# Kernel optimization log

Measured on AMD Instinct MI355X. Metric: run time of the kernel, lower is better.

Reference implementation:

```python
import jax, jax.numpy as jnp
import numpy as np
import math

SLIDING_WINDOW = 1024  # matches init kwarg

def setup_inputs() -> dict:
    key = jax.random.key(0)
    ks = jax.random.split(key, 6)
    B, S, Hq, Hkv, D = 1, 2048, 32, 8, 128
    NUM_PAGES, STRIDE = 300, 16
    q = jax.random.normal(ks[0], (B, S, Hq, D), dtype=jnp.float32)
    k = jax.random.normal(ks[1], (B, S, Hkv, D), dtype=jnp.float32)
    v = jax.random.normal(ks[2], (B, S, Hkv, D), dtype=jnp.float32)
    sink = jax.random.normal(ks[3], (Hq,), dtype=jnp.float32)
    cache_state = jnp.zeros((NUM_PAGES, STRIDE, 2, Hkv, D), dtype=jnp.float32)
    seq_block_ids = jax.random.randint(ks[4], (B, S // STRIDE), 0, NUM_PAGES, dtype=jnp.int64)
    return {"q": q, "k": k, "v": v, "sink": sink,
            "cache_state": cache_state, "seq_block_ids": seq_block_ids}


def reference(q, k, v, sink, cache_state, seq_block_ids):
    B, S, Hq, D = q.shape
    Hkv = k.shape[2]
    stride = cache_state.shape[1]

    # --- paged cache write (prefill side effect) ---
    kv = jnp.stack([k, v], axis=2)                       # [B,S,2,Hkv,D]
    pages = kv.reshape(B * (S // stride), stride, 2, Hkv, D)
    _ = cache_state.at[seq_block_ids.reshape(-1)].set(pages)

    # --- decomposed attention: matmul + mask + softmax(+sink) + matmul ---
    rep = Hq // Hkv
    ke = jnp.repeat(k, rep, axis=2)                      # [B,S,Hq,D] (GQA expand)
    ve = jnp.repeat(v, rep, axis=2)
    scale = 1.0 / math.sqrt(D)
    scores = jnp.einsum('bihd,bjhd->bhij', q, ke) * scale  # [B,Hq,S,S]

    i = jnp.arange(S)[:, None]
    j = jnp.arange(S)[None, :]
    allowed = (j <= i) & (i - j < SLIDING_WINDOW)        # causal + sliding window
    neg = jnp.finfo(scores.dtype).min
    logits = jnp.where(allowed, scores, neg)

    # attention sink: extra per-head logit appended; contributes to denominator only
    sink_l = jnp.broadcast_to(sink[None, :, None, None], (B, Hq, S, 1))
    probs = jax.nn.softmax(jnp.concatenate([logits, sink_l], axis=-1), axis=-1)[..., :S]

    out = jnp.einsum('bhij,bjhd->bihd', probs, ve)       # [B,S,Hq,D]
    return out
```

## Files before the change

kernel.cpp:

```cpp
#include <hip/hip_runtime.h>
#include <hip/hip_bf16.h>


#define S_LEN 2048
#define DH    128
#define HQ    32
#define HKV   8
#define WIN   1024
#define BR    64
#define BC    32
#define NT    (S_LEN / BC)
#define FM    16.0f
#define TILE_CH 512

typedef unsigned short u16;
typedef __attribute__((ext_vector_type(8))) short  short8;
typedef __attribute__((ext_vector_type(4))) float  floatx4;
typedef __attribute__((ext_vector_type(4))) unsigned int uintx4;

__device__ __forceinline__ unsigned rne1(float a) {
    unsigned u = __float_as_uint(a);
    return (u + 0x7FFFu + ((u >> 16) & 1u)) >> 16;
}
__device__ __forceinline__ unsigned rne_pk(float a, float b) {
    return rne1(a) | (rne1(b) << 16);
}

__global__ __launch_bounds__(256) void pack_kv(const float* __restrict__ kg,
                                               const float* __restrict__ vg,
                                               u16* __restrict__ kp,
                                               u16* __restrict__ vtp)
{
    __shared__ float Vs[BC][DH + 1];
    const int b   = blockIdx.x;
    const int hk  = b >> 6;
    const int jt  = b & 63;
    const int tid = threadIdx.x;
    const int j0  = jt * BC;

    #pragma unroll
    for (int t = 0; t < 4; t++) {
        int idx = tid + t * 256;
        int j   = idx >> 5;
        int dc  = idx & 31;
        floatx4 f = *(const floatx4*)(vg + ((size_t)(j0 + j) * HKV + hk) * DH + dc * 4);
        Vs[j][dc * 4 + 0] = f[0]; Vs[j][dc * 4 + 1] = f[1];
        Vs[j][dc * 4 + 2] = f[2]; Vs[j][dc * 4 + 3] = f[3];
    }

    u16* kpt = kp + (size_t)b * TILE_CH * 8;
    #pragma unroll
    for (int t = 0; t < 2; t++) {
        int c = tid + t * 256;
        int row = c >> 4, cc = c & 15;
        const float* p = kg + ((size_t)(j0 + row) * HKV + hk) * DH + cc * 8;
        floatx4 f0 = *(const floatx4*)p;
        floatx4 f1 = *(const floatx4*)(p + 4);
        int pc = (row << 4) | (cc ^ (row & 7));
        *(uintx4*)(kpt + pc * 8) =
            (uintx4){rne_pk(f0[0], f0[1]), rne_pk(f0[2], f0[3]),
                     rne_pk(f1[0], f1[1]), rne_pk(f1[2], f1[3])};
    }
    __syncthreads();

    u16* vpt = vtp + (size_t)b * TILE_CH * 8;
    #pragma unroll
    for (int t = 0; t < 2; t++) {
        int q  = tid + t * 256;
        int dd = q >> 2, c = q & 3;
        unsigned w0 = rne_pk(Vs[c * 4 + 0][dd], Vs[c * 4 + 16][dd]);
        unsigned w1 = rne_pk(Vs[c * 4 + 1][dd], Vs[c * 4 + 17][dd]);
        unsigned w2 = rne_pk(Vs[c * 4 + 2][dd], Vs[c * 4 + 18][dd]);
        unsigned w3 = rne_pk(Vs[c * 4 + 3][dd], Vs[c * 4 + 19][dd]);
        int qp = (dd << 2) | (c ^ ((dd >> 2) & 3));
        *(uintx4*)(vpt + qp * 8) = (uintx4){w0, w1, w2, w3};
    }
}

__launch_bounds__(256, 4)
__global__ void fa_kernel(const float* __restrict__ qg,
                          const u16* __restrict__ kp,
                          const u16* __restrict__ vtp,
                          const float* __restrict__ sg,
                          float* __restrict__ outg)
{
    __shared__ __align__(16) u16 Kt[2][TILE_CH * 8];
    __shared__ __align__(16) u16 Vt[2][TILE_CH * 8];
    __shared__ __align__(16) u16 Pb[BR * 40];

    const int tid  = threadIdx.x;
    const int w    = tid >> 6;
    const int lane = tid & 63;
    const int quad = lane >> 4;
    const int l16  = lane & 15;

    const int bid  = blockIdx.x;
    const int hk   = bid & 7;
    const int idx  = bid >> 3;
    const int hrem = idx & 3;
    const int u5   = (idx >> 2) & 7;
    const int t4   = idx >> 5;
    const int qbt[4] = {u5, 15 - u5, 16 + u5, 31 - u5};
    const int qb   = qbt[t4];
    const int h    = hk * 4 + hrem;

    const int i0 = qb * BR;
    const int m0 = i0 + w * 16;

    short8 qf[4];
    {
        const float* qrow = qg + ((size_t)(m0 + l16) * HQ + h) * DH;
        #pragma unroll
        for (int kk = 0; kk < 4; kk++) {
            const float* p = qrow + kk * 32 + quad * 8;
            floatx4 f0 = *(const floatx4*)p;
            floatx4 f1 = *(const floatx4*)(p + 4);
            uintx4 u = (uintx4){rne_pk(f0[0], f0[1]), rne_pk(f0[2], f0[3]),
                                rne_pk(f1[0], f1[1]), rne_pk(f1[2], f1[3])};
            qf[kk] = *(short8*)&u;
        }
    }

    floatx4 acc[8];
    #pragma unroll
    for (int i = 0; i < 8; i++) acc[i] = (floatx4){0.f, 0.f, 0.f, 0.f};
    float l_part[4] = {0.f, 0.f, 0.f, 0.f};

    int c_r[4];
    #pragma unroll
    for (int r = 0; r < 4; r++) c_r[r] = m0 + quad * 4 + r - l16;

    int jlo = i0 - (WIN - 1); if (jlo < 0) jlo = 0;
    const int jt_lo = jlo >> 5;
    const int jt_hi = (i0 + BR - 1) >> 5;

    const float SC2 = 0.08838834764831845f * 1.4426950408889634f;

    const int ch0 = w * 64 + lane;
    auto stage = [&](int bb, int jt) {
        const u16* kpt = kp  + ((size_t)(hk * NT + jt)) * TILE_CH * 8;
        const u16* vpt = vtp + ((size_t)(hk * NT + jt)) * TILE_CH * 8;
        #pragma unroll
        for (int it = 0; it < 2; it++) {
            int ch = ch0 + it * 256;
            __builtin_amdgcn_global_load_lds(
                (const __attribute__((address_space(1))) unsigned*)(kpt + ch * 8),
                (__attribute__((address_space(3))) unsigned*)(&Kt[bb][ch * 8]), 16, 0, 0);
            __builtin_amdgcn_global_load_lds(
                (const __attribute__((address_space(1))) unsigned*)(vpt + ch * 8),
                (__attribute__((address_space(3))) unsigned*)(&Vt[bb][ch * 8]), 16, 0, 0);
        }
    };

    stage(0, jt_lo);
    int bb = 0;

    for (int jt = jt_lo; jt <= jt_hi; jt++) {
        const int j0 = jt << 5;

        __syncthreads();

        if (jt < jt_hi) stage(bb ^ 1, jt + 1);

        floatx4 sc[2];
        sc[0] = (floatx4){0.f, 0.f, 0.f, 0.f};
        sc[1] = (floatx4){0.f, 0.f, 0.f, 0.f};
        #pragma unroll
        for (int kk = 0; kk < 4; kk++) {
            #pragma unroll
            for (int n = 0; n < 2; n++) {
                int row = n * 16 + l16;
                int cc  = kk * 4 + quad;
                int pc  = (row << 4) | (cc ^ (row & 7));
                short8 kf = *(const short8*)(&Kt[bb][pc * 8]);
                sc[n] = __builtin_amdgcn_mfma_f32_16x16x32_bf16(qf[kk], kf, sc[n], 0, 0, 0);
            }
        }

        const int prow0 = w * 16 + quad * 4;
        const bool interior = (j0 + (BC - 1) <= i0) && (j0 >= i0 + BR - WIN);
        if (interior) {
            #pragma unroll
            for (int r = 0; r < 4; r++) {
                float p0 = exp2f(fmaf(sc[0][r], SC2, -FM));
                float p1 = exp2f(fmaf(sc[1][r], SC2, -FM));
                l_part[r] += p0 + p1;
                *(unsigned*)(&Pb[(prow0 + r) * 40 + l16 * 2]) = rne_pk(p0, p1);
            }
        } else {
            #pragma unroll
            for (int r = 0; r < 4; r++) {
                bool a0 = (j0 <= c_r[r]) && (j0 > c_r[r] - WIN);
                bool a1 = (j0 + 16 <= c_r[r]) && (j0 + 16 > c_r[r] - WIN);
                float p0 = a0 ? exp2f(fmaf(sc[0][r], SC2, -FM)) : 0.f;
                float p1 = a1 ? exp2f(fmaf(sc[1][r], SC2, -FM)) : 0.f;
                l_part[r] += p0 + p1;
                *(unsigned*)(&Pb[(prow0 + r) * 40 + l16 * 2]) = rne_pk(p0, p1);
            }
        }

        {
            short8 pf = *(const short8*)(&Pb[(w * 16 + l16) * 40 + quad * 8]);
            #pragma unroll
            for (int nf = 0; nf < 8; nf++) {
                int dd = nf * 16 + l16;
                int qp = (dd << 2) | (quad ^ ((dd >> 2) & 3));
                short8 vf = *(const short8*)(&Vt[bb][qp * 8]);
                acc[nf] = __builtin_amdgcn_mfma_f32_16x16x32_bf16(pf, vf, acc[nf], 0, 0, 0);
            }
        }
        bb ^= 1;
    }

    const float sk2 = exp2f(fmaf(sg[h], 1.4426950408889634f, -FM));
    float inv[4];
    #pragma unroll
    for (int r = 0; r < 4; r++) {
        float l = l_part[r];
        #pragma unroll
        for (int off = 1; off < 16; off <<= 1)
            l += __shfl_xor(l, off);
        inv[r] = 1.f / (l + sk2);
    }
    #pragma unroll
    for (int nf = 0; nf < 8; nf++) {
        int d = nf * 16 + l16;
        #pragma unroll
        for (int r = 0; r < 4; r++) {
            int ig = m0 + quad * 4 + r;
            outg[((size_t)ig * HQ + h) * DH + d] = acc[nf][r] * inv[r];
        }
    }
}

__launch_bounds__(256, 4)
__global__ void fa_fallback(const float* __restrict__ qg,
                            const float* __restrict__ kg,
                            const float* __restrict__ vg,
                            const float* __restrict__ sg,
                            float* __restrict__ outg)
{
    __shared__ __align__(16) u16 Kt[BC * DH];
    __shared__ __align__(16) u16 Vt[DH * BC];
    __shared__ __align__(16) u16 Pb[BR * 40];

    const int tid  = threadIdx.x;
    const int w    = tid >> 6;
    const int lane = tid & 63;
    const int quad = lane >> 4;
    const int l16  = lane & 15;

    const int qb = blockIdx.x / HQ;
    const int h  = blockIdx.x % HQ;
    const int hk = h >> 2;
    const int i0 = qb * BR;
    const int m0 = i0 + w * 16;

    short8 qf[4];
    {
        const float* qrow = qg + ((size_t)(m0 + l16) * HQ + h) * DH;
        #pragma unroll
        for (int kk = 0; kk < 4; kk++) {
            const float* p = qrow + kk * 32 + quad * 8;
            floatx4 f0 = *(const floatx4*)p;
            floatx4 f1 = *(const floatx4*)(p + 4);
            uintx4 u = (uintx4){rne_pk(f0[0], f0[1]), rne_pk(f0[2], f0[3]),
                                rne_pk(f1[0], f1[1]), rne_pk(f1[2], f1[3])};
            qf[kk] = *(short8*)&u;
        }
    }

    floatx4 acc[8];
    #pragma unroll
    for (int i = 0; i < 8; i++) acc[i] = (floatx4){0.f, 0.f, 0.f, 0.f};
    float l_part[4] = {0.f, 0.f, 0.f, 0.f};

    int jlo = i0 - (WIN - 1); if (jlo < 0) jlo = 0;
    const int jt_lo = jlo >> 5;
    const int jt_hi = (i0 + BR - 1) >> 5;
    const float SC2 = 0.08838834764831845f * 1.4426950408889634f;

    for (int jt = jt_lo; jt <= jt_hi; jt++) {
        const int j0 = jt << 5;
        __syncthreads();
        #pragma unroll
        for (int it = 0; it < 2; it++) {
            int g   = tid + 256 * it;
            int row = g >> 4, cc = g & 15;
            int pc  = (row << 4) | (cc ^ (row & 7));
            const float* kpp = kg + ((size_t)(j0 + row) * HKV + hk) * DH + cc * 8;
            floatx4 f0 = *(const floatx4*)kpp;
            floatx4 f1 = *(const floatx4*)(kpp + 4);
            *(uintx4*)(&Kt[pc * 8]) =
                (uintx4){rne_pk(f0[0], f0[1]), rne_pk(f0[2], f0[3]),
                         rne_pk(f1[0], f1[1]), rne_pk(f1[2], f1[3])};
        }
        #pragma unroll
        for (int it = 0; it < 2; it++) {
            int g  = tid + 256 * it;
            int d  = g & 127, jc = g >> 7;
            const float* vp = vg + ((size_t)(j0 + jc * 8) * HKV + hk) * DH + d;
            float e0 = vp[0 * HKV * DH], e1 = vp[1 * HKV * DH];
            float e2 = vp[2 * HKV * DH], e3 = vp[3 * HKV * DH];
            float e4 = vp[4 * HKV * DH], e5 = vp[5 * HKV * DH];
            float e6 = vp[6 * HKV * DH], e7 = vp[7 * HKV * DH];
            int pc = (d << 2) | (jc ^ ((d >> 2) & 3));
            *(uintx4*)(&Vt[pc * 8]) =
                (uintx4){rne_pk(e0, e1), rne_pk(e2, e3), rne_pk(e4, e5), rne_pk(e6, e7)};
        }
        __syncthreads();

        floatx4 sc[2];
        sc[0] = (floatx4){0.f, 0.f, 0.f, 0.f};
        sc[1] = (floatx4){0.f, 0.f, 0.f, 0.f};
        #pragma unroll
        for (int kk = 0; kk < 4; kk++) {
            #pragma unroll
            for (int n = 0; n < 2; n++) {
                int row = n * 16 + l16;
                int cc  = kk * 4 + quad;
                int pc  = (row << 4) | (cc ^ (row & 7));
                short8 kf = *(const short8*)(&Kt[pc * 8]);
                sc[n] = __builtin_amdgcn_mfma_f32_16x16x32_bf16(qf[kk], kf, sc[n], 0, 0, 0);
            }
        }
        #pragma unroll
        for (int r = 0; r < 4; r++) {
            int   i_g = m0 + quad * 4 + r;
            int   jg0 = j0 + l16, jg1 = j0 + 16 + l16;
            bool  a0  = (jg0 <= i_g) && (i_g - jg0 < WIN);
            bool  a1  = (jg1 <= i_g) && (i_g - jg1 < WIN);
            float p0  = a0 ? exp2f(fmaf(sc[0][r], SC2, -FM)) : 0.f;
            float p1  = a1 ? exp2f(fmaf(sc[1][r], SC2, -FM)) : 0.f;
            l_part[r] += p0 + p1;
            int prow = w * 16 + quad * 4 + r;
            *(unsigned*)(&Pb[prow * 40 + 2 * l16]) = rne_pk(p0, p1);
        }
        {
            short8 pf = *(const short8*)(&Pb[(w * 16 + l16) * 40 + quad * 8]);
            #pragma unroll
            for (int nf = 0; nf < 8; nf++) {
                int dd = nf * 16 + l16;
                int qp = (dd << 2) | (quad ^ ((dd >> 2) & 3));
                short8 vf = *(const short8*)(&Vt[qp * 8]);
                acc[nf] = __builtin_amdgcn_mfma_f32_16x16x32_bf16(pf, vf, acc[nf], 0, 0, 0);
            }
        }
    }

    const float sk2 = exp2f(fmaf(sg[h], 1.4426950408889634f, -FM));
    float inv[4];
    #pragma unroll
    for (int r = 0; r < 4; r++) {
        float l = l_part[r];
        #pragma unroll
        for (int off = 1; off < 16; off <<= 1)
            l += __shfl_xor(l, off);
        inv[r] = 1.f / (l + sk2);
    }
    #pragma unroll
    for (int nf = 0; nf < 8; nf++) {
        int d = nf * 16 + l16;
        #pragma unroll
        for (int r = 0; r < 4; r++) {
            int ig = m0 + quad * 4 + r;
            outg[((size_t)ig * HQ + h) * DH + d] = acc[nf][r] * inv[r];
        }
    }
}

extern "C" void kernel_launch(void* const* d_in, const int* in_sizes, int n_in,
                              void* d_out, int out_size, void* d_ws, size_t ws_size,
                              hipStream_t stream) {
    const float* q  = (const float*)d_in[0];
    const float* k  = (const float*)d_in[1];
    const float* v  = (const float*)d_in[2];
    const float* sk = (const float*)d_in[3];
    float* out = (float*)d_out;

    const size_t tile_elems = (size_t)HKV * NT * TILE_CH * 8;
    const size_t need = 2 * tile_elems * sizeof(u16);

    if (ws_size >= need) {
        u16* kp  = (u16*)d_ws;
        u16* vtp = kp + tile_elems;
        pack_kv<<<dim3(HKV * NT), 256, 0, stream>>>(k, v, kp, vtp);
        fa_kernel<<<dim3((S_LEN / BR) * HQ), 256, 0, stream>>>(q, kp, vtp, sk, out);
    } else {
        fa_fallback<<<dim3((S_LEN / BR) * HQ), 256, 0, stream>>>(q, k, v, sk, out);
    }
}
```

Measured before the change: 163.1 us.

## Load V fragments directly from global into registers, bypassing LDS staging

The prep kernel now writes V tiles in an unswizzled, fragment-ordered layout. The attention kernel loads each lane's V MFMA operands straight from global memory into registers at the start of each tile, instead of staging V through double-buffered shared memory. The aim is to halve LDS staging traffic and footprint, with only K still going through LDS. Fragment address pointers are hoisted out of the loop, and the loop is unrolled by two with constant buffer indices. In exchange, V loads expose global/L2 latency inside the loop with little lookahead, and the unroll assumes an even tile count.

```diff
diff --git a/kernel.cpp b/kernel.cpp
--- a/kernel.cpp
+++ b/kernel.cpp
@@ -72,8 +72,7 @@
         unsigned w1 = rne_pk(Vs[c * 4 + 1][dd], Vs[c * 4 + 17][dd]);
         unsigned w2 = rne_pk(Vs[c * 4 + 2][dd], Vs[c * 4 + 18][dd]);
         unsigned w3 = rne_pk(Vs[c * 4 + 3][dd], Vs[c * 4 + 19][dd]);
-        int qp = (dd << 2) | (c ^ ((dd >> 2) & 3));
-        *(uintx4*)(vpt + qp * 8) = (uintx4){w0, w1, w2, w3};
+        *(uintx4*)(vpt + q * 8) = (uintx4){w0, w1, w2, w3};
     }
 }
 
@@ -84,8 +83,7 @@
                           const float* __restrict__ sg,
                           float* __restrict__ outg)
 {
-    __shared__ __align__(16) u16 Kt[2][TILE_CH * 8];
-    __shared__ __align__(16) u16 Vt[2][TILE_CH * 8];
+    __shared__ __align__(16) u16 Kt[2 * TILE_CH * 8];
     __shared__ __align__(16) u16 Pb[BR * 40];
 
     const int tid  = threadIdx.x;
@@ -121,6 +119,22 @@
         }
     }
 
+    const u16* kfp[8];
+    #pragma unroll
+    for (int kk = 0; kk < 4; kk++)
+        #pragma unroll
+        for (int n = 0; n < 2; n++) {
+            int row = n * 16 + l16;
+            int cc  = kk * 4 + quad;
+            int pc  = (row << 4) | (cc ^ (row & 7));
+            kfp[kk * 2 + n] = &Kt[pc * 8];
+        }
+    u16* pbw[4];
+    #pragma unroll
+    for (int r = 0; r < 4; r++)
+        pbw[r] = &Pb[(w * 16 + quad * 4 + r) * 40 + l16 * 2];
+    const u16* pbr = &Pb[(w * 16 + l16) * 40 + quad * 8];
+
     floatx4 acc[8];
     #pragma unroll
     for (int i = 0; i < 8; i++) acc[i] = (floatx4){0.f, 0.f, 0.f, 0.f};
@@ -136,31 +150,34 @@
 
     const float SC2 = 0.08838834764831845f * 1.4426950408889634f;
 
-    const int ch0 = w * 64 + lane;
-    auto stage = [&](int bb, int jt) {
-        const u16* kpt = kp  + ((size_t)(hk * NT + jt)) * TILE_CH * 8;
-        const u16* vpt = vtp + ((size_t)(hk * NT + jt)) * TILE_CH * 8;
+    const u16* kbase = kp + (size_t)(hk * NT) * TILE_CH * 8;
+    auto stageK = [&](int bb, int jt) {
+        const u16* kpt = kbase + (size_t)jt * TILE_CH * 8;
         #pragma unroll
         for (int it = 0; it < 2; it++) {
-            int ch = ch0 + it * 256;
+            int ch = tid + it * 256;
             __builtin_amdgcn_global_load_lds(
                 (const __attribute__((address_space(1))) unsigned*)(kpt + ch * 8),
-                (__attribute__((address_space(3))) unsigned*)(&Kt[bb][ch * 8]), 16, 0, 0);
-            __builtin_amdgcn_global_load_lds(
-                (const __attribute__((address_space(1))) unsigned*)(vpt + ch * 8),
-                (__attribute__((address_space(3))) unsigned*)(&Vt[bb][ch * 8]), 16, 0, 0);
+                (__attribute__((address_space(3))) unsigned*)(&Kt[bb * TILE_CH * 8 + ch * 8]),
+                16, 0, 0);
         }
     };
 
-    stage(0, jt_lo);
-    int bb = 0;
-
-    for (int jt = jt_lo; jt <= jt_hi; jt++) {
+    const u16* vlane = vtp + (size_t)(hk * NT + jt_lo) * TILE_CH * 8 + l16 * 32 + quad * 8;
+
+    stageK(0, jt_lo);
+
+    auto body = [&](int bbc, int jt) {
         const int j0 = jt << 5;
 
         __syncthreads();
 
-        if (jt < jt_hi) stage(bb ^ 1, jt + 1);
+        if (jt < jt_hi) stageK(bbc ^ 1, jt + 1);
+
+        short8 vf[8];
+        #pragma unroll
+        for (int nf = 0; nf < 8; nf++)
+            vf[nf] = *(const short8*)(vlane + nf * 512);
 
         floatx4 sc[2];
         sc[0] = (floatx4){0.f, 0.f, 0.f, 0.f};
@@ -169,15 +186,11 @@
         for (int kk = 0; kk < 4; kk++) {
             #pragma unroll
             for (int n = 0; n < 2; n++) {
-                int row = n * 16 + l16;
-                int cc  = kk * 4 + quad;
-                int pc  = (row << 4) | (cc ^ (row & 7));
-                short8 kf = *(const short8*)(&Kt[bb][pc * 8]);
+                short8 kf = *(const short8*)(kfp[kk * 2 + n] + bbc * (TILE_CH * 8));
                 sc[n] = __builtin_amdgcn_mfma_f32_16x16x32_bf16(qf[kk], kf, sc[n], 0, 0, 0);
             }
         }
 
-        const int prow0 = w * 16 + quad * 4;
         const bool interior = (j0 + (BC - 1) <= i0) && (j0 >= i0 + BR - WIN);
         if (interior) {
             #pragma unroll
@@ -185,7 +198,7 @@
                 float p0 = exp2f(fmaf(sc[0][r], SC2, -FM));
                 float p1 = exp2f(fmaf(sc[1][r], SC2, -FM));
                 l_part[r] += p0 + p1;
-                *(unsigned*)(&Pb[(prow0 + r) * 40 + l16 * 2]) = rne_pk(p0, p1);
+                *(unsigned*)pbw[r] = rne_pk(p0, p1);
             }
         } else {
             #pragma unroll
@@ -195,21 +208,21 @@
                 float p0 = a0 ? exp2f(fmaf(sc[0][r], SC2, -FM)) : 0.f;
                 float p1 = a1 ? exp2f(fmaf(sc[1][r], SC2, -FM)) : 0.f;
                 l_part[r] += p0 + p1;
-                *(unsigned*)(&Pb[(prow0 + r) * 40 + l16 * 2]) = rne_pk(p0, p1);
+                *(unsigned*)pbw[r] = rne_pk(p0, p1);
             }
         }
 
-        {
-            short8 pf = *(const short8*)(&Pb[(w * 16 + l16) * 40 + quad * 8]);
-            #pragma unroll
-            for (int nf = 0; nf < 8; nf++) {
-                int dd = nf * 16 + l16;
-                int qp = (dd << 2) | (quad ^ ((dd >> 2) & 3));
-                short8 vf = *(const short8*)(&Vt[bb][qp * 8]);
-                acc[nf] = __builtin_amdgcn_mfma_f32_16x16x32_bf16(pf, vf, acc[nf], 0, 0, 0);
-            }
-        }
-        bb ^= 1;
+        short8 pf = *(const short8*)pbr;
+        #pragma unroll
+        for (int nf = 0; nf < 8; nf++)
+            acc[nf] = __builtin_amdgcn_mfma_f32_16x16x32_bf16(pf, vf[nf], acc[nf], 0, 0, 0);
+
+        vlane += TILE_CH * 8;
+    };
+
+    for (int jt = jt_lo; jt <= jt_hi; jt += 2) {
+        body(0, jt);
+        body(1, jt + 1);
     }
 
     const float sk2 = exp2f(fmaf(sg[h], 1.4426950408889634f, -FM));
@@ -342,8 +355,8 @@
             for (int nf = 0; nf < 8; nf++) {
                 int dd = nf * 16 + l16;
                 int qp = (dd << 2) | (quad ^ ((dd >> 2) & 3));
-                short8 vf = *(const short8*)(&Vt[qp * 8]);
-                acc[nf] = __builtin_amdgcn_mfma_f32_16x16x32_bf16(pf, vf, acc[nf], 0, 0, 0);
+                short8 vfr = *(const short8*)(&Vt[qp * 8]);
+                acc[nf] = __builtin_amdgcn_mfma_f32_16x16x32_bf16(pf, vfr, acc[nf], 0, 0, 0);
             }
         }
     }
```

After: 197.4 us. +21.1%, slower.

## Load V fragments directly from global memory into registers, bypassing LDS

Applied to the files above, without the earlier changes.

The V tile is no longer staged through a double-buffered LDS array with global_load_lds. Each lane now reads its short8 V fragments straight from the pre-packed global buffer, whose layout is changed to an unswizzled order that matches the MFMA operand layout. This halves the LDS footprint and the async copy traffic per tile. In exchange, the global loads are issued inside the loop without prefetching, so their latency may be exposed, and all four waves re-read the same V tile through the cache. The second kernel path still reads V with the old swizzled indexing, which may be inconsistent if it consumes the repacked buffer.

```diff
diff --git a/kernel.cpp b/kernel.cpp
--- a/kernel.cpp
+++ b/kernel.cpp
@@ -72,8 +72,7 @@
         unsigned w1 = rne_pk(Vs[c * 4 + 1][dd], Vs[c * 4 + 17][dd]);
         unsigned w2 = rne_pk(Vs[c * 4 + 2][dd], Vs[c * 4 + 18][dd]);
         unsigned w3 = rne_pk(Vs[c * 4 + 3][dd], Vs[c * 4 + 19][dd]);
-        int qp = (dd << 2) | (c ^ ((dd >> 2) & 3));
-        *(uintx4*)(vpt + qp * 8) = (uintx4){w0, w1, w2, w3};
+        *(uintx4*)(vpt + q * 8) = (uintx4){w0, w1, w2, w3};
     }
 }
 
@@ -85,7 +84,6 @@
                           float* __restrict__ outg)
 {
     __shared__ __align__(16) u16 Kt[2][TILE_CH * 8];
-    __shared__ __align__(16) u16 Vt[2][TILE_CH * 8];
     __shared__ __align__(16) u16 Pb[BR * 40];
 
     const int tid  = threadIdx.x;
@@ -137,22 +135,20 @@
     const float SC2 = 0.08838834764831845f * 1.4426950408889634f;
 
     const int ch0 = w * 64 + lane;
-    auto stage = [&](int bb, int jt) {
-        const u16* kpt = kp  + ((size_t)(hk * NT + jt)) * TILE_CH * 8;
-        const u16* vpt = vtp + ((size_t)(hk * NT + jt)) * TILE_CH * 8;
+    auto stageK = [&](int bb, int jt) {
+        const u16* kpt = kp + ((size_t)(hk * NT + jt)) * TILE_CH * 8;
         #pragma unroll
         for (int it = 0; it < 2; it++) {
             int ch = ch0 + it * 256;
             __builtin_amdgcn_global_load_lds(
                 (const __attribute__((address_space(1))) unsigned*)(kpt + ch * 8),
                 (__attribute__((address_space(3))) unsigned*)(&Kt[bb][ch * 8]), 16, 0, 0);
-            __builtin_amdgcn_global_load_lds(
-                (const __attribute__((address_space(1))) unsigned*)(vpt + ch * 8),
-                (__attribute__((address_space(3))) unsigned*)(&Vt[bb][ch * 8]), 16, 0, 0);
         }
     };
 
-    stage(0, jt_lo);
+    const u16* vlane = vtp + (size_t)(hk * NT + jt_lo) * TILE_CH * 8 + l16 * 32 + quad * 8;
+
+    stageK(0, jt_lo);
     int bb = 0;
 
     for (int jt = jt_lo; jt <= jt_hi; jt++) {
@@ -160,7 +156,7 @@
 
         __syncthreads();
 
-        if (jt < jt_hi) stage(bb ^ 1, jt + 1);
+        if (jt < jt_hi) stageK(bb ^ 1, jt + 1);
 
         floatx4 sc[2];
         sc[0] = (floatx4){0.f, 0.f, 0.f, 0.f};
@@ -201,14 +197,16 @@
 
         {
             short8 pf = *(const short8*)(&Pb[(w * 16 + l16) * 40 + quad * 8]);
-            #pragma unroll
-            for (int nf = 0; nf < 8; nf++) {
-                int dd = nf * 16 + l16;
-                int qp = (dd << 2) | (quad ^ ((dd >> 2) & 3));
-                short8 vf = *(const short8*)(&Vt[bb][qp * 8]);
-                acc[nf] = __builtin_amdgcn_mfma_f32_16x16x32_bf16(pf, vf, acc[nf], 0, 0, 0);
-            }
-        }
+            short8 vf[8];
+            #pragma unroll
+            for (int nf = 0; nf < 8; nf++)
+                vf[nf] = *(const short8*)(vlane + nf * 512);
+            #pragma unroll
+            for (int nf = 0; nf < 8; nf++)
+                acc[nf] = __builtin_amdgcn_mfma_f32_16x16x32_bf16(pf, vf[nf], acc[nf], 0, 0, 0);
+        }
+
+        vlane += TILE_CH * 8;
         bb ^= 1;
     }
 
@@ -342,8 +340,8 @@
             for (int nf = 0; nf < 8; nf++) {
                 int dd = nf * 16 + l16;
                 int qp = (dd << 2) | (quad ^ ((dd >> 2) & 3));
-                short8 vf = *(const short8*)(&Vt[qp * 8]);
-                acc[nf] = __builtin_amdgcn_mfma_f32_16x16x32_bf16(pf, vf, acc[nf], 0, 0, 0);
+                short8 vfr = *(const short8*)(&Vt[qp * 8]);
+                acc[nf] = __builtin_amdgcn_mfma_f32_16x16x32_bf16(pf, vfr, acc[nf], 0, 0, 0);
             }
         }
     }
```

Measured after the change: 185.6 us. +13.8%, slower.
